# Optimization experiments

Hardware: AMD Instinct MI355X
Metric: run time of the kernel (lower is better)

Reference implementation:

```python
import jax, jax.numpy as jnp
import numpy as np

ORDER = 7
ALPHA = 1.0
BETA = 1.0

def _jacobi_coeffs(order, a, b):
    k1 = np.zeros(order + 1, dtype=np.float32)
    k2 = np.zeros(order + 1, dtype=np.float32)
    k3 = np.zeros(order + 1, dtype=np.float32)
    for i in range(2, order + 1):
        k1[i] = (2*i + a + b) * (2*i + a + b - 1) / (2*i * (i + a + b))
        k2[i] = (2*i + a + b - 1) * (a*a - b*b) / (2*i * (i + a + b) * (2*i + a + b - 2))
        k3[i] = (i + a - 1) * (i + b - 1) * (2*i + a + b) / (i * (i + a + b) * (2*i + a + b - 2))
    return k1, k2, k3

K1, K2, K3 = _jacobi_coeffs(ORDER, ALPHA, BETA)

def setup_inputs() -> dict:
    key = jax.random.key(0)
    kx, kc = jax.random.split(key)
    batch, input_size, output_size = 4096, 512, 512
    x = jax.random.normal(kx, (batch, input_size), dtype=jnp.float32)
    coef = jax.random.normal(kc, (output_size, input_size, ORDER + 1), dtype=jnp.float32) * 0.1
    return {"x": x, "coef": coef}

def _precompute_jacobi(x):
    # x: [B, I] -> jacobi values [B, I, order+1]
    x = jnp.tanh(x)
    p0 = jnp.ones_like(x)
    p1 = 0.5 * (ALPHA + BETA + 2.0) * x - 0.5 * (ALPHA - BETA)
    vals = [p0, p1]
    for i in range(2, ORDER + 1):
        vals.append((K1[i] * x + K2[i]) * vals[i - 1] - K3[i] * vals[i - 2])
    return jnp.stack(vals, axis=2)  # [B, I, D]

def reference(x, coef):
    jac = _precompute_jacobi(x)                 # [B, I, D]
    # sum_j over input and order dims in one contraction
    return jnp.einsum('bid,jid->bj', jac, coef)  # [B, O]
```

## Files before the change

kernel.cpp:

```cpp
#include <hip/hip_runtime.h>
#include <stdint.h>

#define BATCH 4096
#define ISZ   512
#define OSZ   512
#define KDIM  4096

#define TM 128
#define TN 128
#define BK 64
#define SPLITK 4

typedef __bf16 bf16x8 __attribute__((ext_vector_type(8)));
typedef float  f32x4  __attribute__((ext_vector_type(4)));

__device__ __forceinline__ unsigned short f2bf(float f) {
    uint32_t u = __float_as_uint(f);
    u = (u + 0x7FFFu + ((u >> 16) & 1u)) >> 16;
    return (unsigned short)u;
}

#define NB_CONV 2048
#define NB_JAC  2048
__global__ __launch_bounds__(256) void prep(
    const float* __restrict__ coef, unsigned short* __restrict__ coefb,
    const float* __restrict__ X,    unsigned short* __restrict__ Ab)
{
    const int b = blockIdx.x;
    if (b < NB_CONV) {
        int idx = b * 256 + threadIdx.x;
        float4 v = reinterpret_cast<const float4*>(coef)[idx];
        uint2 o;
        o.x = (uint32_t)f2bf(v.x) | ((uint32_t)f2bf(v.y) << 16);
        o.y = (uint32_t)f2bf(v.z) | ((uint32_t)f2bf(v.w) << 16);
        reinterpret_cast<uint2*>(coefb)[idx] = o;
    } else {
        int idx = (b - NB_CONV) * 256 + threadIdx.x;
        float4 xv = reinterpret_cast<const float4*>(X)[idx];
        const float xs[4] = {xv.x, xv.y, xv.z, xv.w};
        #pragma unroll
        for (int j = 0; j < 4; ++j) {
            float e  = __expf(2.0f * xs[j]);
            float t  = 1.0f - 2.0f * __builtin_amdgcn_rcpf(e + 1.0f);
            float p0 = 1.0f;
            float p1 = 2.0f * t;
            float p2 = (1.875f     * t) * p1 - 0.75f       * p0;
            float p3 = (1.8666667f * t) * p2 - 0.8f        * p1;
            float p4 = (1.875f     * t) * p3 - 0.83333333f * p2;
            float p5 = (1.8857143f * t) * p4 - 0.85714287f * p3;
            float p6 = (1.8958333f * t) * p5 - 0.875f      * p4;
            float p7 = (1.9047619f * t) * p6 - 0.88888889f * p5;
            uint4 o;
            o.x = (uint32_t)f2bf(p0) | ((uint32_t)f2bf(p1) << 16);
            o.y = (uint32_t)f2bf(p2) | ((uint32_t)f2bf(p3) << 16);
            o.z = (uint32_t)f2bf(p4) | ((uint32_t)f2bf(p5) << 16);
            o.w = (uint32_t)f2bf(p6) | ((uint32_t)f2bf(p7) << 16);
            reinterpret_cast<uint4*>(Ab)[idx * 4 + j] = o;
        }
    }
}

__global__ __launch_bounds__(256, 2) void gemm_fused(
    const unsigned short* __restrict__ Am,
    const unsigned short* __restrict__ Bm,
    unsigned short* __restrict__ Cp,
    int M, int N, int K)
{
    __shared__ __align__(16) unsigned short As[2][TM * BK];
    __shared__ __align__(16) unsigned short Bs[2][TN * BK];

    const int tid  = threadIdx.x;
    const int wave = tid >> 6;
    const int lane = tid & 63;
    const int wm   = (wave >> 1) * 64;
    const int wn   = (wave & 1) * 64;

    const size_t baseA = (size_t)blockIdx.x * TM * K;
    const size_t baseB = (size_t)blockIdx.y * TN * K;
    const int kper  = K / SPLITK;
    const int kbeg  = blockIdx.z * kper;
    const int niter = kper / BK;

    f32x4 acc[4][4] = {};

    const int mrow = lane & 15;
    const int kc   = lane >> 4;

    auto stage = [&](const unsigned short* __restrict__ G, size_t gbase,
                     unsigned short* lds, int k0) {
        #pragma unroll
        for (int it = 0; it < 4; ++it) {
            int s    = it * 256 + tid;
            int row  = s >> 3;
            int csrc = (s & 7) ^ (row & 7);
            const unsigned short* g = G + gbase + (size_t)row * K + k0 + csrc * 8;
            unsigned short* l = lds + (size_t)(it * 256 + wave * 64) * 8;
            __builtin_amdgcn_global_load_lds(
                (const __attribute__((address_space(1))) uint32_t*)g,
                (__attribute__((address_space(3))) uint32_t*)l, 16, 0, 0);
        }
    };

    stage(Bm, baseB, &Bs[0][0], kbeg);
    stage(Am, baseA, &As[0][0], kbeg);
    __syncthreads();

    for (int kt = 0; kt < niter; ++kt) {
        const int k0 = kbeg + kt * BK;
        const int p  = kt & 1;
        if (kt + 1 < niter) {
            stage(Bm, baseB, &Bs[1 - p][0], k0 + BK);
            stage(Am, baseA, &As[1 - p][0], k0 + BK);
        }

        const unsigned short* Ap = &As[p][0];
        const unsigned short* Bp = &Bs[p][0];
        #pragma unroll
        for (int ks = 0; ks < BK; ks += 32) {
            bf16x8 aF[4], bF[4];
            const int cbase = (ks >> 3) + kc;
            #pragma unroll
            for (int mi = 0; mi < 4; ++mi) {
                int r = wm + mi * 16 + mrow;
                int slot = r * 8 + (cbase ^ (r & 7));
                aF[mi] = *reinterpret_cast<const bf16x8*>(Ap + (size_t)slot * 8);
            }
            #pragma unroll
            for (int ni = 0; ni < 4; ++ni) {
                int r = wn + ni * 16 + mrow;
                int slot = r * 8 + (cbase ^ (r & 7));
                bF[ni] = *reinterpret_cast<const bf16x8*>(Bp + (size_t)slot * 8);
            }
            #pragma unroll
            for (int mi = 0; mi < 4; ++mi)
                #pragma unroll
                for (int ni = 0; ni < 4; ++ni)
                    acc[mi][ni] = __builtin_amdgcn_mfma_f32_16x16x32_bf16(
                        aF[mi], bF[ni], acc[mi][ni], 0, 0, 0);
        }
        __syncthreads();
    }

    unsigned short* Cz = Cp + (size_t)blockIdx.z * M * N;
    const int orow = blockIdx.x * TM + wm + (lane >> 4) * 4;
    const int ocol = blockIdx.y * TN + wn + (lane & 15);
    #pragma unroll
    for (int mi = 0; mi < 4; ++mi)
        #pragma unroll
        for (int ni = 0; ni < 4; ++ni)
            #pragma unroll
            for (int r = 0; r < 4; ++r)
                Cz[(size_t)(orow + mi * 16 + r) * N + ocol + ni * 16] =
                    f2bf(acc[mi][ni][r]);
}

__global__ __launch_bounds__(256) void reduce_k(
    const unsigned short* __restrict__ part, float* __restrict__ out, int n8)
{
    int idx = blockIdx.x * 256 + threadIdx.x;
    if (idx >= n8) return;
    const uint4* p = reinterpret_cast<const uint4*>(part);
    float s[8] = {};
    #pragma unroll
    for (int z = 0; z < SPLITK; ++z) {
        uint4 v = p[(size_t)z * n8 + idx];
        s[0] += __uint_as_float((v.x & 0xFFFFu) << 16);
        s[1] += __uint_as_float(v.x & 0xFFFF0000u);
        s[2] += __uint_as_float((v.y & 0xFFFFu) << 16);
        s[3] += __uint_as_float(v.y & 0xFFFF0000u);
        s[4] += __uint_as_float((v.z & 0xFFFFu) << 16);
        s[5] += __uint_as_float(v.z & 0xFFFF0000u);
        s[6] += __uint_as_float((v.w & 0xFFFFu) << 16);
        s[7] += __uint_as_float(v.w & 0xFFFF0000u);
    }
    float4 o0 = {s[0], s[1], s[2], s[3]};
    float4 o1 = {s[4], s[5], s[6], s[7]};
    reinterpret_cast<float4*>(out)[2 * idx]     = o0;
    reinterpret_cast<float4*>(out)[2 * idx + 1] = o1;
}

extern "C" void kernel_launch(void* const* d_in, const int* in_sizes, int n_in,
                              void* d_out, int out_size, void* d_ws, size_t ws_size,
                              hipStream_t stream)
{
    const float* x    = (const float*)d_in[0];
    const float* coef = (const float*)d_in[1];
    float* out = (float*)d_out;

    unsigned short* part  = (unsigned short*)d_ws;
    unsigned short* coefb = part  + (size_t)SPLITK * BATCH * OSZ;
    unsigned short* Ab    = coefb + (size_t)OSZ * KDIM;

    prep<<<NB_CONV + NB_JAC, 256, 0, stream>>>(coef, coefb, x, Ab);

    dim3 grid(BATCH / TM, OSZ / TN, SPLITK);
    gemm_fused<<<grid, 256, 0, stream>>>(Ab, coefb, part, BATCH, OSZ, KDIM);

    int n8r = (BATCH * OSZ) / 8;
    reduce_k<<<(n8r + 255) / 256, 256, 0, stream>>>(part, out, n8r);
}
```

Baseline: 102.2 us.

## Fuse split-K reduction into GEMM via per-tile atomic counter

Removes the separate reduce kernel by having each split-K block increment a per-tile atomic counter after writing its bf16 partial; the last block for a tile sums all partials and writes fp32 output. Counters are zeroed in the prep kernel. This saves a kernel launch and a full pass over the partial buffer, at the cost of threadfences, an atomic per block, and serialized reduction work in the last-arriving blocks.

```diff
diff --git a/kernel.cpp b/kernel.cpp
--- a/kernel.cpp
+++ b/kernel.cpp
@@ -10,6 +10,8 @@
 #define TN 128
 #define BK 64
 #define SPLITK 4
+#define NTILEY (OSZ / TN)
+#define NTILES ((BATCH / TM) * NTILEY)
 
 typedef __bf16 bf16x8 __attribute__((ext_vector_type(8)));
 typedef float  f32x4  __attribute__((ext_vector_type(4)));
@@ -24,9 +26,11 @@
 #define NB_JAC  2048
 __global__ __launch_bounds__(256) void prep(
     const float* __restrict__ coef, unsigned short* __restrict__ coefb,
-    const float* __restrict__ X,    unsigned short* __restrict__ Ab)
+    const float* __restrict__ X,    unsigned short* __restrict__ Ab,
+    int* __restrict__ cnt)
 {
     const int b = blockIdx.x;
+    if (b == 0 && threadIdx.x < NTILES) cnt[threadIdx.x] = 0;
     if (b < NB_CONV) {
         int idx = b * 256 + threadIdx.x;
         float4 v = reinterpret_cast<const float4*>(coef)[idx];
@@ -64,6 +68,8 @@
     const unsigned short* __restrict__ Am,
     const unsigned short* __restrict__ Bm,
     unsigned short* __restrict__ Cp,
+    float* __restrict__ Out,
+    int* __restrict__ cnt,
     int M, int N, int K)
 {
     __shared__ __align__(16) unsigned short As[2][TM * BK];
@@ -152,31 +158,42 @@
             for (int r = 0; r < 4; ++r)
                 Cz[(size_t)(orow + mi * 16 + r) * N + ocol + ni * 16] =
                     f2bf(acc[mi][ni][r]);
-}
-
-__global__ __launch_bounds__(256) void reduce_k(
-    const unsigned short* __restrict__ part, float* __restrict__ out, int n8)
-{
-    int idx = blockIdx.x * 256 + threadIdx.x;
-    if (idx >= n8) return;
-    const uint4* p = reinterpret_cast<const uint4*>(part);
-    float s[8] = {};
-    #pragma unroll
-    for (int z = 0; z < SPLITK; ++z) {
-        uint4 v = p[(size_t)z * n8 + idx];
-        s[0] += __uint_as_float((v.x & 0xFFFFu) << 16);
-        s[1] += __uint_as_float(v.x & 0xFFFF0000u);
-        s[2] += __uint_as_float((v.y & 0xFFFFu) << 16);
-        s[3] += __uint_as_float(v.y & 0xFFFF0000u);
-        s[4] += __uint_as_float((v.z & 0xFFFFu) << 16);
-        s[5] += __uint_as_float(v.z & 0xFFFF0000u);
-        s[6] += __uint_as_float((v.w & 0xFFFFu) << 16);
-        s[7] += __uint_as_float(v.w & 0xFFFF0000u);
+
+    __threadfence();
+    __syncthreads();
+    __shared__ int sPrev;
+    const int tileId = blockIdx.x * NTILEY + blockIdx.y;
+    if (tid == 0) sPrev = atomicAdd(&cnt[tileId], 1);
+    __syncthreads();
+    if (sPrev == SPLITK - 1) {
+        __threadfence();
+        const int row0 = blockIdx.x * TM;
+        const int col0 = blockIdx.y * TN;
+        #pragma unroll
+        for (int rr = 0; rr < 8; ++rr) {
+            const int row = (tid >> 4) + rr * 16;
+            const int col = (tid & 15) * 8;
+            const size_t off = (size_t)(row0 + row) * N + col0 + col;
+            float s[8] = {};
+            #pragma unroll
+            for (int z = 0; z < SPLITK; ++z) {
+                uint4 v = *reinterpret_cast<const uint4*>(
+                    Cp + (size_t)z * M * N + off);
+                s[0] += __uint_as_float((v.x & 0xFFFFu) << 16);
+                s[1] += __uint_as_float(v.x & 0xFFFF0000u);
+                s[2] += __uint_as_float((v.y & 0xFFFFu) << 16);
+                s[3] += __uint_as_float(v.y & 0xFFFF0000u);
+                s[4] += __uint_as_float((v.z & 0xFFFFu) << 16);
+                s[5] += __uint_as_float(v.z & 0xFFFF0000u);
+                s[6] += __uint_as_float((v.w & 0xFFFFu) << 16);
+                s[7] += __uint_as_float(v.w & 0xFFFF0000u);
+            }
+            float4 o0 = {s[0], s[1], s[2], s[3]};
+            float4 o1 = {s[4], s[5], s[6], s[7]};
+            *reinterpret_cast<float4*>(Out + off)     = o0;
+            *reinterpret_cast<float4*>(Out + off + 4) = o1;
+        }
     }
-    float4 o0 = {s[0], s[1], s[2], s[3]};
-    float4 o1 = {s[4], s[5], s[6], s[7]};
-    reinterpret_cast<float4*>(out)[2 * idx]     = o0;
-    reinterpret_cast<float4*>(out)[2 * idx + 1] = o1;
 }
 
 extern "C" void kernel_launch(void* const* d_in, const int* in_sizes, int n_in,
@@ -190,12 +207,11 @@
     unsigned short* part  = (unsigned short*)d_ws;
     unsigned short* coefb = part  + (size_t)SPLITK * BATCH * OSZ;
     unsigned short* Ab    = coefb + (size_t)OSZ * KDIM;
-
-    prep<<<NB_CONV + NB_JAC, 256, 0, stream>>>(coef, coefb, x, Ab);
+    int*            cnt   = (int*)(Ab + (size_t)BATCH * KDIM);
+
+    prep<<<NB_CONV + NB_JAC, 256, 0, stream>>>(coef, coefb, x, Ab, cnt);
 
     dim3 grid(BATCH / TM, OSZ / TN, SPLITK);
-    gemm_fused<<<grid, 256, 0, stream>>>(Ab, coefb, part, BATCH, OSZ, KDIM);
-
-    int n8r = (BATCH * OSZ) / 8;
-    reduce_k<<<(n8r + 255) / 256, 256, 0, stream>>>(part, out, n8r);
-}
+    gemm_fused<<<grid, 256, 0, stream>>>(Ab, coefb, part, out, cnt,
+                                         BATCH, OSZ, KDIM);
+}
```

Result: slower. 176.2 us (+72.5%).
